# Kernel optimization log

Hardware: AMD Instinct MI355X
Metric: run time of the kernel (lower is better)

## Reference

```python
import jax, jax.numpy as jnp
import numpy as np
import math

FILT = 5
CENTER = FILT / 2 - 0.5          # filtSide/2 - 0.5 from calculate_weights
LN_E = math.log(2.71828)         # real(2.71828**(i*t)) == cos(t*ln(2.71828))
CUTOFF = math.sqrt(CENTER * CENTER + 0.25)
OUT_CH, IN_CH = 16, 8


def _zernike_tables(out_ch, in_ch):
    """Replicates the (n, m) index walk and the polys() coefficients."""
    K = out_ch * in_ch
    n, m = 2, 0
    ns, ms = [], []
    for _ in range(K):
        if m == n:
            n += 1
            m = 0
        else:
            m += 1
        ns.append(n)
        ms.append(m)
    S = max(1, max((nn - mm) // 2 for nn, mm in zip(ns, ms)))
    C = np.zeros((K, S), np.float64)   # top/bot coefficient per (pair, s)
    E = np.zeros((K, S), np.int32)     # exponent n - 2s per (pair, s)
    for p, (nn, mm) in enumerate(zip(ns, ms)):
        for s in range((nn - mm) // 2):
            top = (-1) ** s * math.factorial(nn - s)
            bot = (math.factorial(s)
                   * math.gamma((nn + mm) / 2 - s + 1)
                   * math.gamma((nn - mm) / 2 - s) + 1)
            C[p, s] = top / bot
            E[p, s] = nn - 2 * s
    return C.astype(np.float32), E, np.array(ns, np.int32)


def setup_inputs() -> dict:
    key = jax.random.key(0)
    B, H, W = 8, 1024, 1024
    x = jax.random.normal(key, (B, IN_CH, H, W), dtype=jnp.float32)
    C, E, N = _zernike_tables(OUT_CH, IN_CH)
    return {
        "x": x,
        "coeff": jnp.asarray(C),           # [K, S] float32
        "expn": jnp.asarray(E),            # [K, S] int32
        "nvals": jnp.asarray(N),           # [K]    int32
    }


def _zernike_weights(coeff, expn, nvals):
    # kernel grid geometry (radialDist)
    ii = jnp.arange(FILT, dtype=jnp.float32)[:, None]
    jj = jnp.arange(FILT, dtype=jnp.float32)[None, :]
    a = jnp.abs(ii - CENTER)
    b = jnp.abs(jj - CENTER)
    dist = jnp.sqrt(a * a + b * b)
    radial = jnp.where(dist <= CUTOFF, dist, 0.0)          # [5,5]
    rsafe = jnp.where(radial > 0, radial, 1.0)             # avoid 0**0 / grad NaNs
    # polys: poly[p,i,j] = sum_s C[p,s] * r^(n-2s), only where radial>0
    terms = coeff[:, :, None, None] * rsafe[None, None] ** expn[:, :, None, None].astype(jnp.float32)
    poly = jnp.where(radial > 0, jnp.sum(terms, axis=1), 0.0)   # [K,5,5]
    # expo: multiply by real(2.71828**(i*n*phi)) only where poly>0
    phi = jnp.arctan(b / (a + 0.001))                      # [5,5]
    cosr = jnp.cos(nvals[:, None, None].astype(jnp.float32) * phi * LN_E)
    w = jnp.where(poly > 0, poly * cosr, poly)
    return w.reshape(OUT_CH, IN_CH, FILT, FILT)


def reference(x, coeff, expn, nvals):
    w = _zernike_weights(coeff, expn, nvals)
    return jax.lax.conv_general_dilated(
        x, w,
        window_strides=(1, 1),
        padding=((2, 2), (2, 2)),
        dimension_numbers=("NCHW", "OIHW", "NCHW"),
    )
```

## Files before the change

### kernel.cpp

```cpp
#include <hip/hip_runtime.h>


typedef __attribute__((ext_vector_type(8))) short bf16x8;
typedef __attribute__((ext_vector_type(4))) float f32x4;

#define OUT_CH 16
#define IN_CH  8
#define FILT   5
#define NTAPS  28
#define IMG    1024
#define TH     16
#define TW     64
#define LR     (TH + 4)
#define LC     72
#define CGRP   (LC / 4)

static __device__ __forceinline__ unsigned short f32_to_bf16_rne(float f) {
    unsigned int u = __float_as_uint(f);
    u = u + 0x7fffu + ((u >> 16) & 1u);
    return (unsigned short)(u >> 16);
}
static __device__ __forceinline__ float bf16_bits_to_f32(unsigned short h) {
    return __uint_as_float(((unsigned int)h) << 16);
}
static __device__ __forceinline__ unsigned int pk2(float lo, float hi) {
    return (unsigned int)f32_to_bf16_rne(lo) |
           ((unsigned int)f32_to_bf16_rne(hi) << 16);
}

__global__ void zernike_weights_kernel(const float* __restrict__ coeff,
                                       const int* __restrict__ expn,
                                       const int* __restrict__ nvals,
                                       int K, int S,
                                       unsigned short* __restrict__ whi,
                                       unsigned short* __restrict__ wlo) {
    int idx = blockIdx.x * blockDim.x + threadIdx.x;
    if (idx >= K * NTAPS) return;
    int p   = idx / NTAPS;
    int tap = idx - p * NTAPS;
    const float CENTER = 2.0f;
    const float CUTOFF = sqrtf(4.25f);
    const float LNE    = 0.99999932734f;
    int co = p >> 3, ci = p & 7;
    float nv = (float)nvals[p];

    float w = 0.0f;
    if (tap < 25) {
        int i = tap / 5, j = tap % 5;
        float a = fabsf((float)i - CENTER);
        float b = fabsf((float)j - CENTER);
        float dist = sqrtf(a * a + b * b);
        float radial = (dist <= CUTOFF) ? dist : 0.0f;
        float rsafe = (radial > 0.0f) ? radial : 1.0f;
        float poly = 0.0f;
        for (int s = 0; s < S; ++s) {
            float C = coeff[p * S + s];
            int   e = expn[p * S + s];
            float pw = 1.0f;
            for (int t = 0; t < e; ++t) pw *= rsafe;
            poly += C * pw;
        }
        if (!(radial > 0.0f)) poly = 0.0f;
        float phi  = atanf(b / (a + 0.001f));
        float cosr = cosf(nv * phi * LNE);
        w = (poly > 0.0f) ? poly * cosr : poly;
    }
    unsigned short hi = f32_to_bf16_rne(w);
    unsigned short lo = f32_to_bf16_rne(w - bf16_bits_to_f32(hi));
    int oidx = (co * NTAPS + tap) * 8 + ci;
    whi[oidx] = hi;
    wlo[oidx] = lo;
}

__global__ __launch_bounds__(256) void conv_mfma_kernel(
        const float* __restrict__ x,
        const unsigned short* __restrict__ whi,
        const unsigned short* __restrict__ wlo,
        float* __restrict__ out) {
    __shared__ uint4 tile[LR * LC];

    const int tx   = blockIdx.x * TW;
    const int ty   = blockIdx.y * TH;
    const int b    = blockIdx.z;
    const int tid  = threadIdx.x;
    const int lane = tid & 63;
    const int wv   = tid >> 6;
    const int quad = lane >> 4;
    const int n15  = lane & 15;

    bf16x8 a_hi[7], a_lo[7];
#pragma unroll
    for (int q = 0; q < 7; ++q) {
        int tap = q * 4 + quad;
        int off = (n15 * NTAPS + tap) * 8;
        a_hi[q] = *(const bf16x8*)(whi + off);
        a_lo[q] = *(const bf16x8*)(wlo + off);
    }

    const float* xb = x + (((long)b * IN_CH) << 20);
    for (int g = tid; g < LR * CGRP; g += 256) {
        int r   = g / CGRP;
        int cg  = g - r * CGRP;
        int gy  = ty + r - 2;
        int gx0 = tx + (cg << 2) - 4;
        uint4 u[4];
        if (((unsigned)gy < IMG) & ((unsigned)gx0 < IMG)) {
            const float* px = xb + (gy << 10) + gx0;
            f32x4 v[8];
#pragma unroll
            for (int ci = 0; ci < 8; ++ci)
                v[ci] = *(const f32x4*)(px + (ci << 20));
#pragma unroll
            for (int j = 0; j < 4; ++j) {
                u[j].x = pk2(v[0][j], v[1][j]);
                u[j].y = pk2(v[2][j], v[3][j]);
                u[j].z = pk2(v[4][j], v[5][j]);
                u[j].w = pk2(v[6][j], v[7][j]);
            }
        } else {
#pragma unroll
            for (int j = 0; j < 4; ++j) {
                u[j].x = 0u; u[j].y = 0u; u[j].z = 0u; u[j].w = 0u;
            }
        }
        int t0 = r * LC + (cg << 2);
#pragma unroll
        for (int j = 0; j < 4; ++j) tile[t0 + j] = u[j];
    }
    __syncthreads();

    int offq[7];
#pragma unroll
    for (int q = 0; q < 7; ++q) {
        int tap = q * 4 + quad;
        int kh = (tap < 25) ? (tap / 5) : 0;
        int kw = (tap < 25) ? (tap % 5) : 0;
        offq[q] = kh * LC + kw + 2;
    }

    const int row0 = wv * 4;
#pragma unroll
    for (int gr = 0; gr < 4; ++gr) {
        int row = row0 + gr;
#pragma unroll
        for (int gc = 0; gc < 4; ++gc) {
            int c0   = gc * 16;
            int base = row * LC + c0 + n15;
            f32x4 acc_h = {0.f, 0.f, 0.f, 0.f};
            f32x4 acc_l = {0.f, 0.f, 0.f, 0.f};
#pragma unroll
            for (int q = 0; q < 7; ++q) {
                bf16x8 bfrag = *(const bf16x8*)&tile[base + offq[q]];
                acc_h = __builtin_amdgcn_mfma_f32_16x16x32_bf16(a_hi[q], bfrag, acc_h, 0, 0, 0);
                acc_l = __builtin_amdgcn_mfma_f32_16x16x32_bf16(a_lo[q], bfrag, acc_l, 0, 0, 0);
            }
            int gy  = ty + row;
            int gxp = tx + c0 + n15;
#pragma unroll
            for (int r = 0; r < 4; ++r) {
                int co = quad * 4 + r;
                out[(((b * OUT_CH + co) << 10) + gy << 10) + gxp] = acc_h[r] + acc_l[r];
            }
        }
    }
}

extern "C" void kernel_launch(void* const* d_in, const int* in_sizes, int n_in,
                              void* d_out, int out_size, void* d_ws, size_t ws_size,
                              hipStream_t stream) {
    const float* x     = (const float*)d_in[0];
    const float* coeff = (const float*)d_in[1];
    const int*   expn  = (const int*)d_in[2];
    const int*   nvals = (const int*)d_in[3];
    int K = in_sizes[3];
    int S = in_sizes[1] / K;

    unsigned short* whi = (unsigned short*)d_ws;
    unsigned short* wlo = whi + OUT_CH * NTAPS * 8;

    int wthreads = K * NTAPS;
    zernike_weights_kernel<<<(wthreads + 255) / 256, 256, 0, stream>>>(
        coeff, expn, nvals, K, S, whi, wlo);

    dim3 grid(IMG / TW, IMG / TH, 8);
    conv_mfma_kernel<<<grid, 256, 0, stream>>>(x, whi, wlo, (float*)d_out);
}
```

Measured before the change: 806.2 us.

## Pre-convert input to bf16 NHWC and stage tiles via global_load_lds

Adds a separate pass that converts the fp32 NCHW input into packed bf16 channels-last pixels in workspace. The conv kernel then fills its LDS tile with direct global-to-LDS 16-byte loads, using a zeroed workspace slot for padding. This removes the per-block conversion and register staging in the conv. The cost is an extra full read of the input plus a write and re-read of the converted copy.

```diff
diff --git a/kernel.cpp b/kernel.cpp
--- a/kernel.cpp
+++ b/kernel.cpp
@@ -6,14 +6,17 @@
 
 #define OUT_CH 16
 #define IN_CH  8
-#define FILT   5
 #define NTAPS  28
 #define IMG    1024
 #define TH     16
 #define TW     64
 #define LR     (TH + 4)
-#define LC     72
-#define CGRP   (LC / 4)
+#define LC     (TW + 4)
+#define NPIX   (LR * LC)
+#define NPIXP  1536
+
+#define GLOBAL_AS __attribute__((address_space(1)))
+#define LDS_AS    __attribute__((address_space(3)))
 
 static __device__ __forceinline__ unsigned short f32_to_bf16_rne(float f) {
     unsigned int u = __float_as_uint(f);
@@ -33,8 +36,10 @@
                                        const int* __restrict__ nvals,
                                        int K, int S,
                                        unsigned short* __restrict__ whi,
-                                       unsigned short* __restrict__ wlo) {
+                                       unsigned short* __restrict__ wlo,
+                                       unsigned int* __restrict__ zeropad) {
     int idx = blockIdx.x * blockDim.x + threadIdx.x;
+    if (blockIdx.x == 0 && threadIdx.x < 16) zeropad[threadIdx.x] = 0u;
     if (idx >= K * NTAPS) return;
     int p   = idx / NTAPS;
     int tap = idx - p * NTAPS;
@@ -72,12 +77,36 @@
     wlo[oidx] = lo;
 }
 
+__global__ __launch_bounds__(256) void cvt_nhwc_kernel(
+        const float* __restrict__ x, uint4* __restrict__ xp) {
+    const int t   = threadIdx.x;
+    const int row = blockIdx.x;
+    const float* px = x + (((long)(row >> 10)) << 23)
+                        + ((long)(row & 1023) << 10);
+    const int px0 = t << 2;
+    f32x4 v[8];
+#pragma unroll
+    for (int ci = 0; ci < 8; ++ci)
+        v[ci] = *(const f32x4*)(px + ((long)ci << 20) + px0);
+    uint4* dst = xp + (((long)row << 10) + px0);
+#pragma unroll
+    for (int j = 0; j < 4; ++j) {
+        uint4 u;
+        u.x = pk2(v[0][j], v[1][j]);
+        u.y = pk2(v[2][j], v[3][j]);
+        u.z = pk2(v[4][j], v[5][j]);
+        u.w = pk2(v[6][j], v[7][j]);
+        dst[j] = u;
+    }
+}
+
 __global__ __launch_bounds__(256) void conv_mfma_kernel(
-        const float* __restrict__ x,
+        const uint4* __restrict__ xp,
+        const uint4* __restrict__ zsrc,
         const unsigned short* __restrict__ whi,
         const unsigned short* __restrict__ wlo,
         float* __restrict__ out) {
-    __shared__ uint4 tile[LR * LC];
+    __shared__ uint4 tile[NPIXP];
 
     const int tx   = blockIdx.x * TW;
     const int ty   = blockIdx.y * TH;
@@ -97,35 +126,18 @@
         a_lo[q] = *(const bf16x8*)(wlo + off);
     }
 
-    const float* xb = x + (((long)b * IN_CH) << 20);
-    for (int g = tid; g < LR * CGRP; g += 256) {
-        int r   = g / CGRP;
-        int cg  = g - r * CGRP;
-        int gy  = ty + r - 2;
-        int gx0 = tx + (cg << 2) - 4;
-        uint4 u[4];
-        if (((unsigned)gy < IMG) & ((unsigned)gx0 < IMG)) {
-            const float* px = xb + (gy << 10) + gx0;
-            f32x4 v[8];
-#pragma unroll
-            for (int ci = 0; ci < 8; ++ci)
-                v[ci] = *(const f32x4*)(px + (ci << 20));
-#pragma unroll
-            for (int j = 0; j < 4; ++j) {
-                u[j].x = pk2(v[0][j], v[1][j]);
-                u[j].y = pk2(v[2][j], v[3][j]);
-                u[j].z = pk2(v[4][j], v[5][j]);
-                u[j].w = pk2(v[6][j], v[7][j]);
-            }
-        } else {
-#pragma unroll
-            for (int j = 0; j < 4; ++j) {
-                u[j].x = 0u; u[j].y = 0u; u[j].z = 0u; u[j].w = 0u;
-            }
-        }
-        int t0 = r * LC + (cg << 2);
-#pragma unroll
-        for (int j = 0; j < 4; ++j) tile[t0 + j] = u[j];
+#pragma unroll
+    for (int k = 0; k < 6; ++k) {
+        int p  = k * 256 + tid;
+        int r  = p / LC;
+        int c  = p - r * LC;
+        int gy = ty + r - 2;
+        int gx = tx + c - 2;
+        bool inb = (r < LR) & ((unsigned)gy < IMG) & ((unsigned)gx < IMG);
+        const uint4* src = inb ? (xp + ((b << 20) + (gy << 10) + gx)) : zsrc;
+        __builtin_amdgcn_global_load_lds(
+            (GLOBAL_AS const void*)src,
+            (LDS_AS void*)&tile[p], 16, 0, 0);
     }
     __syncthreads();
 
@@ -135,7 +147,7 @@
         int tap = q * 4 + quad;
         int kh = (tap < 25) ? (tap / 5) : 0;
         int kw = (tap < 25) ? (tap % 5) : 0;
-        offq[q] = kh * LC + kw + 2;
+        offq[q] = kh * LC + kw;
     }
 
     const int row0 = wv * 4;
@@ -175,13 +187,17 @@
     int K = in_sizes[3];
     int S = in_sizes[1] / K;
 
-    unsigned short* whi = (unsigned short*)d_ws;
-    unsigned short* wlo = whi + OUT_CH * NTAPS * 8;
+    unsigned short* whi  = (unsigned short*)d_ws;
+    unsigned short* wlo  = whi + OUT_CH * NTAPS * 8;
+    unsigned int*   zpad = (unsigned int*)((char*)d_ws + 16384);
+    uint4*          xp   = (uint4*)((char*)d_ws + 32768);
 
     int wthreads = K * NTAPS;
     zernike_weights_kernel<<<(wthreads + 255) / 256, 256, 0, stream>>>(
-        coeff, expn, nvals, K, S, whi, wlo);
+        coeff, expn, nvals, K, S, whi, wlo, zpad);
+
+    cvt_nhwc_kernel<<<8 * IMG, 256, 0, stream>>>(x, xp);
 
     dim3 grid(IMG / TW, IMG / TH, 8);
-    conv_mfma_kernel<<<grid, 256, 0, stream>>>(x, whi, wlo, (float*)d_out);
-}
+    conv_mfma_kernel<<<grid, 256, 0, stream>>>(xp, (const uint4*)zpad, whi, wlo, (float*)d_out);
+}
```

After: 850.0 us. 5.4% more time.
